# Kernel tuning notes

Hardware: AMD Instinct MI355X
Metric: run time of the kernel (lower is better)

The kernel has to match this reference:

```python
import jax, jax.numpy as jnp
import numpy as np

P = 8          # patch_num_in == patch_num_out
R = 16         # patch_resolution (pixels per patch side)
C = 2          # dim_channel
D = 512        # dim_token
NH = 8         # nhead
DFF = 2048     # dim_feedforward
L = 6          # num_layers
PAIRS = 5      # demo_num
BS = 8
HW = P * R     # 128
S = PAIRS * 2 * P * P  # 640 tokens
EPS = 1e-5


def _patchify(x):
    # x: (N, c, H, W) -> (N, P*P, c*R*R)
    N, c, H, W = x.shape
    x = x.reshape(N, c, P, R, P, R).transpose(0, 2, 4, 1, 3, 5)
    return x.reshape(N, P * P, c * R * R)


def _depatchify(x, c):
    # x: (N, P*P, c*R*R) -> (N, c, P*R, P*R)
    N = x.shape[0]
    x = x.reshape(N, P, P, c, R, R).transpose(0, 3, 1, 4, 2, 5)
    return x.reshape(N, c, P * R, P * R)


def _ln(x, s, b):
    mu = jnp.mean(x, axis=-1, keepdims=True)
    var = jnp.mean(jnp.square(x - mu), axis=-1, keepdims=True)
    return (x - mu) * jax.lax.rsqrt(var + EPS) * s + b


def _block_lowtri_additive_mask(seq_len):
    blk = jnp.arange(seq_len) // (P * P)  # alternating init/end blocks of size P*P
    allowed = blk[:, None] >= blk[None, :]
    return jnp.where(allowed, 0.0, -jnp.inf).astype(jnp.float32)


def setup_inputs() -> dict:
    key = jax.random.key(0)
    ks = jax.random.split(key, 20)
    s = 0.02
    f32 = jnp.float32
    inp = {
        "init": jax.random.normal(ks[0], (BS, PAIRS, C, HW, HW), f32),
        "end": jax.random.normal(ks[1], (BS, PAIRS, C, HW, HW), f32),
        "c_mask": jnp.ones((BS, C), dtype=bool),
        "pre_W": (jax.random.normal(ks[2], (D, C * R * R), f32) * s),
        "pre_b": jnp.zeros((D,), f32),
        "post_W": (jax.random.normal(ks[3], (C * R * R, D), f32) * s),
        "post_b": jnp.zeros((C * R * R,), f32),
        "patch_pos": jax.random.normal(ks[4], (P * P, D), f32),
        "func_pos": jax.random.normal(ks[5], (PAIRS * 2, D), f32),
        "Wqkv": (jax.random.normal(ks[6], (L, 3 * D, D), f32) * s),
        "bqkv": jnp.zeros((L, 3 * D), f32),
        "Wo": (jax.random.normal(ks[7], (L, D, D), f32) * s),
        "bo": jnp.zeros((L, D), f32),
        "ln1_s": jnp.ones((L, D), f32),
        "ln1_b": jnp.zeros((L, D), f32),
        "ln2_s": jnp.ones((L, D), f32),
        "ln2_b": jnp.zeros((L, D), f32),
        "W1": (jax.random.normal(ks[8], (L, DFF, D), f32) * s),
        "b1": jnp.zeros((L, DFF), f32),
        "W2": (jax.random.normal(ks[9], (L, D, DFF), f32) * s),
        "b2": jnp.zeros((L, D), f32),
    }
    return inp


def _forward(init, end, pre_W, pre_b, post_W, post_b, patch_pos, func_pos,
             Wqkv, bqkv, Wo, bo, ln1_s, ln1_b, ln2_s, ln2_b, W1, b1, W2, b2):
    bs, pairs = init.shape[0], init.shape[1]
    # interleave (init, end) per pair: (bs, pairs, 2, c, h, w)
    x = jnp.concatenate([init[:, :, None], end[:, :, None]], axis=2)
    f = x.reshape(-1, C, HW, HW)
    f = _patchify(f)                                    # (N, P*P, C*R*R)
    f = f @ pre_W.T + pre_b                             # (N, P*P, D)
    f = f + patch_pos                                   # patch pos encoding
    f = f.reshape(bs, pairs * 2, P * P, D)
    f = f + func_pos[: pairs * 2][None, :, None, :]     # func pos encoding
    seq = pairs * 2 * P * P
    f = f.reshape(bs, seq, D)

    amask = _block_lowtri_additive_mask(seq)            # (S, S) additive
    dh = D // NH
    scale = 1.0 / np.sqrt(dh).astype(np.float32)

    for l in range(L):
        qkv = f @ Wqkv[l].T + bqkv[l]                   # (bs, S, 3D)
        q, k, v = jnp.split(qkv, 3, axis=-1)
        q = q.reshape(bs, seq, NH, dh).transpose(0, 2, 1, 3)
        k = k.reshape(bs, seq, NH, dh).transpose(0, 2, 1, 3)
        v = v.reshape(bs, seq, NH, dh).transpose(0, 2, 1, 3)
        scores = jnp.einsum('bhqd,bhkd->bhqk', q, k) * scale + amask
        attn = jax.nn.softmax(scores, axis=-1)
        o = jnp.einsum('bhqk,bhkd->bhqd', attn, v)
        o = o.transpose(0, 2, 1, 3).reshape(bs, seq, D)
        o = o @ Wo[l].T + bo[l]
        f = _ln(f + o, ln1_s[l], ln1_b[l])              # post-norm (PyTorch default)
        ff = jax.nn.gelu(f @ W1[l].T + b1[l], approximate=False) @ W2[l].T + b2[l]
        f = _ln(f + ff, ln2_s[l], ln2_b[l])

    f = f.reshape(bs, pairs, 2, P * P, D)[:, :, 0]      # read prediction off init slots
    f = f @ post_W.T + post_b                           # (bs, pairs, P*P, C*R*R)
    f = f.reshape(bs * pairs, P * P, C * R * R)
    f = _depatchify(f, C)
    return f.reshape(bs, pairs, C, HW, HW)


def reference(init, end, c_mask, pre_W, pre_b, post_W, post_b, patch_pos, func_pos,
              Wqkv, bqkv, Wo, bo, ln1_s, ln1_b, ln2_s, ln2_b, W1, b1, W2, b2):
    # c_mask is unpacked but unused by the original forward
    return _forward(init, end, pre_W, pre_b, post_W, post_b, patch_pos, func_pos,
                    Wqkv, bqkv, Wo, bo, ln1_s, ln1_b, ln2_s, ln2_b, W1, b1, W2, b2)
```

## Files before the change

### kernel.cpp

```cpp
#include <hip/hip_runtime.h>
#include <hip/hip_bf16.h>

#define BSZ 8
#define PAIRS 5
#define NCH 2
#define HWP 128
#define PP 64
#define DIM 512
#define NHEAD 8
#define DHEAD 64
#define DFF 2048
#define NLAYER 6
#define SEQ 640
#define NTOK (BSZ * SEQ)
#define FIN 10
#define MPOST (BSZ * PAIRS * PP)

typedef unsigned short u16;
typedef __bf16 bf16_t;
typedef __attribute__((ext_vector_type(8))) __bf16 bf16x8;
typedef __attribute__((ext_vector_type(8))) unsigned short u16x8;
typedef __attribute__((ext_vector_type(4))) unsigned short u16x4;
typedef __attribute__((ext_vector_type(4))) float f32x4;
#define MFMA16(a, b, c) __builtin_amdgcn_mfma_f32_16x16x32_bf16(a, b, c, 0, 0, 0)

__device__ __forceinline__ u16 f2b(float x) {
  unsigned u = __float_as_uint(x);
  return (u16)((u + 0x7fffu + ((u >> 16) & 1u)) >> 16);
}

__device__ __forceinline__ float gelu_t(float x) {
  float y = 0.7978845608f * (x + 0.044715f * x * x * x);
  y = fminf(fmaxf(y, -10.f), 10.f);
  float e = __expf(2.f * y);
  return 0.5f * x * (1.f + (e - 1.f) / (e + 1.f));
}

__device__ __forceinline__ void dma16(const u16* g, void* l) {
  __builtin_amdgcn_global_load_lds(
      (const __attribute__((address_space(1))) void*)g,
      (__attribute__((address_space(3))) void*)l, 16, 0, 0);
}

template <int N> __device__ __forceinline__ void vwait() {
  if constexpr (N == 0) asm volatile("s_waitcnt vmcnt(0)" ::: "memory");
  else if constexpr (N == 2) asm volatile("s_waitcnt vmcnt(2)" ::: "memory");
  else if constexpr (N == 3) asm volatile("s_waitcnt vmcnt(3)" ::: "memory");
  else if constexpr (N == 4) asm volatile("s_waitcnt vmcnt(4)" ::: "memory");
  else if constexpr (N == 6) asm volatile("s_waitcnt vmcnt(6)" ::: "memory");
}

#define W_QKV (3 * DIM * DIM)
#define W_O (DIM * DIM)
#define W_1 (DFF * DIM)
#define OFF_O W_QKV
#define OFF_1 (W_QKV + W_O)
#define OFF_2 (W_QKV + W_O + W_1)
#define W_ALL (W_QKV + W_O + 2 * W_1)
#define PREPOST (2 * DIM * DIM)
#define N_CVT (PREPOST + NLAYER * W_ALL)

__global__ __launch_bounds__(256) void k_cvt_all(const float* __restrict__ preW,
                                                 const float* __restrict__ postW,
                                                 const float* __restrict__ wq,
                                                 const float* __restrict__ wo,
                                                 const float* __restrict__ w1,
                                                 const float* __restrict__ w2,
                                                 u16* __restrict__ dst) {
  size_t i = ((size_t)blockIdx.x * 256 + threadIdx.x) * 8;
  const float* src;
  size_t off;
  if (i < DIM * DIM) { src = preW; off = i; }
  else if (i < PREPOST) { src = postW; off = i - DIM * DIM; }
  else {
    size_t j = i - PREPOST;
    int l = (int)(j / W_ALL);
    size_t r = j - (size_t)l * W_ALL;
    if (r < OFF_O) { src = wq + (size_t)l * W_QKV; off = r; }
    else if (r < OFF_1) { src = wo + (size_t)l * W_O; off = r - OFF_O; }
    else if (r < OFF_2) { src = w1 + (size_t)l * W_1; off = r - OFF_1; }
    else { src = w2 + (size_t)l * W_1; off = r - OFF_2; }
  }
  float4 v0 = *(const float4*)(src + off);
  float4 v1 = *(const float4*)(src + off + 4);
  u16x8 o;
  o[0] = f2b(v0.x); o[1] = f2b(v0.y); o[2] = f2b(v0.z); o[3] = f2b(v0.w);
  o[4] = f2b(v1.x); o[5] = f2b(v1.y); o[6] = f2b(v1.z); o[7] = f2b(v1.w);
  *(u16x8*)(dst + i) = o;
}

__global__ __launch_bounds__(256) void k_patchify(const float* __restrict__ init,
                                                  const float* __restrict__ endp,
                                                  u16* __restrict__ A) {
  int i = blockIdx.x * 256 + threadIdx.x;
  int d = i & 511;
  int g = i >> 9;
  int p = g & 63;
  int fi = (g >> 6) % FIN;
  int b = g / SEQ;
  int e = fi & 1;
  int pr = fi >> 1;
  int c = d >> 8;
  int r1 = (d >> 4) & 15;
  int r2 = d & 15;
  int row = ((p >> 3) << 4) + r1;
  int col = ((p & 7) << 4) + r2;
  const float* src = e ? endp : init;
  size_t off = ((size_t)((b * PAIRS + pr) * NCH + c) << 14) + (size_t)row * HWP + col;
  A[i] = f2b(src[off]);
}

template <int BM, int NT, int MODE, int GATHER>
__global__ __launch_bounds__(256) void k_mma(const u16* __restrict__ A,
                                             const u16* __restrict__ B,
                                             const float* __restrict__ bias,
                                             u16* __restrict__ outB,
                                             float* __restrict__ outP,
                                             float* __restrict__ outF,
                                             const float* __restrict__ pp,
                                             const float* __restrict__ fp,
                                             int M, int N, int K, int act) {
  constexpr int FJ = NT / 32;
  constexpr int MI = BM / 32;
  constexpr int ACH = BM / 16;
  constexpr int NC = (BM / 16 + NT / 16) / 4;
  __shared__ __align__(16) bf16_t As[4][BM][32];
  __shared__ __align__(16) bf16_t Bs[4][NT][32];
  const int t = threadIdx.x;
  const int w = t >> 6, lane = t & 63, quad = lane >> 4, l16 = lane & 15;
  int bx = blockIdx.x, by = blockIdx.y;
  if ((gridDim.y & 7) == 0) {
    int lin = bx + gridDim.x * by;
    int xcd = lin & 7, slot = lin >> 3;
    int gx = gridDim.x;
    by = (gridDim.y >> 3) * xcd + slot / gx;
    bx = slot % gx;
  }
  const int row0 = by * BM, col0 = bx * NT;
  const int mB = (w & 1) * (BM / 2);
  const int nB = (w >> 1) * (NT / 2);

  const u16* aP[ACH];
#pragma unroll
  for (int c = 0; c < ACH; ++c) {
    int r = row0 + c * 16 + (lane >> 2);
    int g = r;
    if (GATHER) {
      int p = r & 63, pr = (r >> 6) % PAIRS, b = r / (PAIRS * PP);
      g = b * SEQ + pr * 128 + p;
    }
    aP[c] = A + (size_t)g * K + ((lane & 3) << 3);
  }
  const u16* bP = B + (size_t)(col0 + (lane >> 2)) * K + ((lane & 3) << 3);

  f32x4 acc[MI][FJ];
#pragma unroll
  for (int i = 0; i < MI; ++i)
#pragma unroll
    for (int j = 0; j < FJ; ++j) acc[i][j] = (f32x4){0.f, 0.f, 0.f, 0.f};

  auto stage = [&](int bu, int kk) {
#pragma unroll
    for (int s = 0; s < NC; ++s) {
      int c = NC * w + s;
      if (c < ACH) dma16(aP[c] + kk, &As[bu][c * 16][0]);
      else dma16(bP + (size_t)((c - ACH) * 16) * K + kk, &Bs[bu][(c - ACH) * 16][0]);
    }
  };

  const int iters = K >> 5;
  stage(0, 0);
  stage(1, 32);
  for (int it = 0; it < iters; ++it) {
    const int cur = it & 3;
    if (it + 2 < iters) stage((it + 2) & 3, (it + 2) << 5);
    if (it + 2 < iters) vwait<2 * NC>();
    else if (it + 1 < iters) vwait<NC>();
    else vwait<0>();
    asm volatile("s_barrier" ::: "memory");
    bf16x8 af[MI], bfr[FJ];
#pragma unroll
    for (int i = 0; i < MI; ++i)
      af[i] = *(const bf16x8*)&As[cur][mB + i * 16 + l16][quad * 8];
#pragma unroll
    for (int j = 0; j < FJ; ++j)
      bfr[j] = *(const bf16x8*)&Bs[cur][nB + j * 16 + l16][quad * 8];
#pragma unroll
    for (int i = 0; i < MI; ++i)
#pragma unroll
      for (int j = 0; j < FJ; ++j) acc[i][j] = MFMA16(af[i], bfr[j], acc[i][j]);
  }

#pragma unroll
  for (int i = 0; i < MI; ++i)
#pragma unroll
    for (int reg = 0; reg < 4; ++reg) {
      int m = row0 + mB + i * 16 + quad * 4 + reg;
#pragma unroll
      for (int j = 0; j < FJ; ++j) {
        int n = col0 + nB + j * 16 + l16;
        float v = acc[i][j][reg];
        if (MODE == 0) {
          v += bias[n];
          if (act) v = gelu_t(v);
          outB[(size_t)m * N + n] = f2b(v);
        } else if (MODE == 1) {
          outP[(size_t)m * N + n] = v;
        } else if (MODE == 2) {
          int p = m & 63, fi = (m >> 6) % FIN;
          v += bias[n] + pp[p * DIM + n] + fp[fi * DIM + n];
          outF[(size_t)m * N + n] = v;
          outB[(size_t)m * N + n] = f2b(v);
        } else {
          v += bias[n];
          int p = m & 63, pr = (m >> 6) % PAIRS, b = m / (PAIRS * PP);
          int c = n >> 8, r1 = (n >> 4) & 15, r2 = n & 15;
          int row = ((p >> 3) << 4) + r1, col = ((p & 7) << 4) + r2;
          size_t off = ((size_t)((b * PAIRS + pr) * NCH + c) << 14) +
                       (size_t)row * HWP + col;
          outF[off] = v;
        }
      }
    }
}

__global__ __launch_bounds__(256) void k_attn(const u16* __restrict__ qkv,
                                              u16* __restrict__ o, int qmul) {
  __shared__ bf16_t Ks[2][64][72];
  __shared__ bf16_t Vs[2][64][72];
  __shared__ bf16_t QPs[64][72];
  const int t = threadIdx.x;
  const int w = t >> 6, lane = t & 63, quad = lane >> 4, l16 = lane & 15;
  const int qblk = ((int)gridDim.x - 1 - (int)blockIdx.x) * qmul;
  const int h = blockIdx.y, b = blockIdx.z;
  const int q0 = qblk << 6;
  const u16* base = qkv + (size_t)b * SEQ * (3 * DIM);
  const int sr = t >> 2;
  const int sd = (t & 3) << 4;
  const int rowB = 3 * DIM;
  const int ntile = qblk + 1;
  {
    const u16* qp = base + (size_t)(q0 + sr) * rowB + h * DHEAD + sd;
    *(bf16x8*)&QPs[sr][sd] = *(const bf16x8*)(const void*)qp;
    *(bf16x8*)&QPs[sr][sd + 8] = *(const bf16x8*)(const void*)(qp + 8);
  }
  const u16* kp0 = base + (size_t)sr * rowB + DIM + h * DHEAD + sd;
  const u16* vp0 = base + (size_t)sr * rowB + 2 * DIM + h * DHEAD + sd;
  bf16x8 kR0 = *(const bf16x8*)(const void*)kp0;
  bf16x8 kR1 = *(const bf16x8*)(const void*)(kp0 + 8);
  bf16x8 vR0 = *(const bf16x8*)(const void*)vp0;
  bf16x8 vR1 = *(const bf16x8*)(const void*)(vp0 + 8);
  *(bf16x8*)&Ks[0][sr][sd] = kR0;
  *(bf16x8*)&Ks[0][sr][sd + 8] = kR1;
#pragma unroll
  for (int e = 0; e < 8; ++e) Vs[0][sd + e][sr] = vR0[e];
#pragma unroll
  for (int e = 0; e < 8; ++e) Vs[0][sd + 8 + e][sr] = vR1[e];
  __syncthreads();
  bf16x8 aQ0 = *(const bf16x8*)&QPs[w * 16 + l16][quad * 8];
  bf16x8 aQ1 = *(const bf16x8*)&QPs[w * 16 + l16][32 + quad * 8];
  f32x4 accO[4];
#pragma unroll
  for (int j = 0; j < 4; ++j) accO[j] = (f32x4){0.f, 0.f, 0.f, 0.f};
  float mSt[4] = {-1e30f, -1e30f, -1e30f, -1e30f};
  float lSt[4] = {0.f, 0.f, 0.f, 0.f};
  for (int kt = 0; kt < ntile; ++kt) {
    const int cur = kt & 1;
    if (kt > 0) __syncthreads();
    if (kt + 1 < ntile) {
      const u16* kp = kp0 + (size_t)(kt + 1) * 64 * rowB;
      const u16* vp = vp0 + (size_t)(kt + 1) * 64 * rowB;
      kR0 = *(const bf16x8*)(const void*)kp;
      kR1 = *(const bf16x8*)(const void*)(kp + 8);
      vR0 = *(const bf16x8*)(const void*)vp;
      vR1 = *(const bf16x8*)(const void*)(vp + 8);
    }
    f32x4 s[4];
#pragma unroll
    for (int j = 0; j < 4; ++j) {
      bf16x8 b0 = *(const bf16x8*)&Ks[cur][j * 16 + l16][quad * 8];
      bf16x8 b1 = *(const bf16x8*)&Ks[cur][j * 16 + l16][32 + quad * 8];
      s[j] = (f32x4){0.f, 0.f, 0.f, 0.f};
      s[j] = MFMA16(aQ0, b0, s[j]);
      s[j] = MFMA16(aQ1, b1, s[j]);
      s[j] *= 0.125f;
    }
#pragma unroll
    for (int reg = 0; reg < 4; ++reg) {
      float mx = fmaxf(fmaxf(s[0][reg], s[1][reg]), fmaxf(s[2][reg], s[3][reg]));
      mx = fmaxf(mx, __shfl_xor(mx, 1));
      mx = fmaxf(mx, __shfl_xor(mx, 2));
      mx = fmaxf(mx, __shfl_xor(mx, 4));
      mx = fmaxf(mx, __shfl_xor(mx, 8));
      float mNew = fmaxf(mSt[reg], mx);
      float alpha = __expf(mSt[reg] - mNew);
      mSt[reg] = mNew;
      float rs = 0.f;
#pragma unroll
      for (int j = 0; j < 4; ++j) {
        float p = __expf(s[j][reg] - mNew);
        s[j][reg] = p;
        rs += p;
      }
      rs += __shfl_xor(rs, 1);
      rs += __shfl_xor(rs, 2);
      rs += __shfl_xor(rs, 4);
      rs += __shfl_xor(rs, 8);
      lSt[reg] = lSt[reg] * alpha + rs;
#pragma unroll
      for (int j = 0; j < 4; ++j) accO[j][reg] *= alpha;
    }
#pragma unroll
    for (int j = 0; j < 4; ++j)
#pragma unroll
      for (int reg = 0; reg < 4; ++reg)
        *(u16*)&QPs[w * 16 + quad * 4 + reg][j * 16 + l16] = f2b(s[j][reg]);
    if (kt + 1 < ntile) {
      const int nxt = cur ^ 1;
      *(bf16x8*)&Ks[nxt][sr][sd] = kR0;
      *(bf16x8*)&Ks[nxt][sr][sd + 8] = kR1;
#pragma unroll
      for (int e = 0; e < 8; ++e) Vs[nxt][sd + e][sr] = vR0[e];
#pragma unroll
      for (int e = 0; e < 8; ++e) Vs[nxt][sd + 8 + e][sr] = vR1[e];
    }
    bf16x8 aP0 = *(const bf16x8*)&QPs[w * 16 + l16][quad * 8];
    bf16x8 aP1 = *(const bf16x8*)&QPs[w * 16 + l16][32 + quad * 8];
#pragma unroll
    for (int jd = 0; jd < 4; ++jd) {
      bf16x8 b0 = *(const bf16x8*)&Vs[cur][jd * 16 + l16][quad * 8];
      bf16x8 b1 = *(const bf16x8*)&Vs[cur][jd * 16 + l16][32 + quad * 8];
      accO[jd] = MFMA16(aP0, b0, accO[jd]);
      accO[jd] = MFMA16(aP1, b1, accO[jd]);
    }
  }
#pragma unroll
  for (int reg = 0; reg < 4; ++reg) {
    float inv = 1.0f / lSt[reg];
    int row = q0 + w * 16 + quad * 4 + reg;
#pragma unroll
    for (int jd = 0; jd < 4; ++jd)
      o[((size_t)(b * SEQ + row)) * DIM + h * DHEAD + jd * 16 + l16] =
          f2b(accO[jd][reg] * inv);
  }
}

template <int GIN>
__global__ __launch_bounds__(256) void k_red_ln(const float* __restrict__ part,
                                                const float* __restrict__ bias,
                                                const float* __restrict__ f_in,
                                                float* __restrict__ f_out,
                                                u16* __restrict__ fb_out,
                                                const float* __restrict__ s,
                                                const float* __restrict__ bvec) {
  const int t = threadIdx.x;
  const int half = t >> 7;
  const int r = blockIdx.x * 2 + half;
  const int c = (t & 127) * 4;
  int g = r;
  if (GIN) {
    int p = r & 63, pr = (r >> 6) % PAIRS, b = r / (PAIRS * PP);
    g = b * SEQ + pr * 128 + p;
  }
  float4 x = *(const float4*)(f_in + (size_t)g * DIM + c);
  float4 pa = *(const float4*)(part + (size_t)r * DIM + c);
  float4 bi = *(const float4*)(bias + c);
  x.x += pa.x + bi.x; x.y += pa.y + bi.y; x.z += pa.z + bi.z; x.w += pa.w + bi.w;
  float sum = x.x + x.y + x.z + x.w;
  float sq = x.x * x.x + x.y * x.y + x.z * x.z + x.w * x.w;
#pragma unroll
  for (int off = 32; off; off >>= 1) {
    sum += __shfl_xor(sum, off);
    sq += __shfl_xor(sq, off);
  }
  __shared__ float rs[4], rq[4];
  const int w = t >> 6, lane = t & 63;
  if (lane == 0) { rs[w] = sum; rq[w] = sq; }
  __syncthreads();
  float tot = rs[half * 2] + rs[half * 2 + 1];
  float tq2 = rq[half * 2] + rq[half * 2 + 1];
  float mu = tot * (1.0f / 512.0f);
  float var = tq2 * (1.0f / 512.0f) - mu * mu;
  float rstd = rsqrtf(var + 1e-5f);
  float4 sv = *(const float4*)(s + c);
  float4 bv = *(const float4*)(bvec + c);
  float4 o;
  o.x = (x.x - mu) * rstd * sv.x + bv.x;
  o.y = (x.y - mu) * rstd * sv.y + bv.y;
  o.z = (x.z - mu) * rstd * sv.z + bv.z;
  o.w = (x.w - mu) * rstd * sv.w + bv.w;
  *(float4*)(f_out + (size_t)r * DIM + c) = o;
  u16x4 ob;
  ob[0] = f2b(o.x); ob[1] = f2b(o.y); ob[2] = f2b(o.z); ob[3] = f2b(o.w);
  *(u16x4*)(fb_out + (size_t)r * DIM + c) = ob;
}

extern "C" void kernel_launch(void* const* d_in, const int* in_sizes, int n_in,
                              void* d_out, int out_size, void* d_ws, size_t ws_size,
                              hipStream_t stream) {
  const float* init = (const float*)d_in[0];
  const float* endp = (const float*)d_in[1];
  const float* pre_W = (const float*)d_in[3];
  const float* pre_b = (const float*)d_in[4];
  const float* post_W = (const float*)d_in[5];
  const float* post_b = (const float*)d_in[6];
  const float* patch_pos = (const float*)d_in[7];
  const float* func_pos = (const float*)d_in[8];
  const float* Wqkv = (const float*)d_in[9];
  const float* bqkv = (const float*)d_in[10];
  const float* Wo = (const float*)d_in[11];
  const float* bo = (const float*)d_in[12];
  const float* ln1_s = (const float*)d_in[13];
  const float* ln1_b = (const float*)d_in[14];
  const float* ln2_s = (const float*)d_in[15];
  const float* ln2_b = (const float*)d_in[16];
  const float* W1 = (const float*)d_in[17];
  const float* b1 = (const float*)d_in[18];
  const float* W2 = (const float*)d_in[19];
  const float* b2 = (const float*)d_in[20];
  float* out = (float*)d_out;

  char* p = (char*)d_ws;
  float* buf_f = (float*)p;    p += (size_t)NTOK * DIM * 4;
  u16* buf_fb = (u16*)p;       p += (size_t)NTOK * DIM * 2;
  u16* buf_attn = (u16*)p;     p += (size_t)NTOK * DIM * 2;
  u16* shared_b = (u16*)p;     p += (size_t)NTOK * DFF * 2;
  u16* wAll = (u16*)p;         p += (size_t)N_CVT * 2;
  float* partial = (float*)p;  p += (size_t)NTOK * DIM * 4;
  float* buf_fc = (float*)p;   p += (size_t)MPOST * DIM * 4;
  u16* buf_fbc = (u16*)p;      p += (size_t)MPOST * DIM * 2;
  u16* buf_patch = shared_b;
  u16* buf_qkv = shared_b;
  u16* buf_hid = shared_b;
  u16* wPre = wAll;
  u16* wPost = wAll + DIM * DIM;
  u16* wL = wAll + PREPOST;

  dim3 blk(256);
  const int elems = NTOK * DIM;

  k_cvt_all<<<N_CVT / (256 * 8), blk, 0, stream>>>(pre_W, post_W, Wqkv, Wo, W1, W2,
                                                   wAll);
  k_patchify<<<elems / 256, blk, 0, stream>>>(init, endp, buf_patch);
  k_mma<64, 64, 2, 0><<<dim3(8, 80), blk, 0, stream>>>(
      buf_patch, wPre, pre_b, buf_fb, nullptr, buf_f, patch_pos, func_pos,
      NTOK, DIM, DIM, 0);

  for (int l = 0; l < NLAYER; ++l) {
    u16* wB = wL + (size_t)l * W_ALL;
    k_mma<64, 128, 0, 0><<<dim3(12, 80), blk, 0, stream>>>(
        buf_fb, wB, bqkv + (size_t)l * 3 * DIM, buf_qkv, nullptr, nullptr, nullptr,
        nullptr, NTOK, 3 * DIM, DIM, 0);
    if (l < NLAYER - 1) {
      k_attn<<<dim3(SEQ / 64, NHEAD, BSZ), blk, 0, stream>>>(buf_qkv, buf_attn, 1);
      k_mma<64, 64, 1, 0><<<dim3(8, 80), blk, 0, stream>>>(
          buf_attn, wB + OFF_O, nullptr, nullptr, partial, nullptr, nullptr, nullptr,
          NTOK, DIM, DIM, 0);
      k_red_ln<0><<<NTOK / 2, blk, 0, stream>>>(partial, bo + (size_t)l * DIM,
                                                buf_f, buf_f, buf_fb,
                                                ln1_s + (size_t)l * DIM,
                                                ln1_b + (size_t)l * DIM);
      k_mma<64, 128, 0, 0><<<dim3(16, 80), blk, 0, stream>>>(
          buf_fb, wB + OFF_1, b1 + (size_t)l * DFF, buf_hid, nullptr, nullptr,
          nullptr, nullptr, NTOK, DFF, DIM, 1);
      k_mma<64, 64, 1, 0><<<dim3(8, 80), blk, 0, stream>>>(
          buf_hid, wB + OFF_2, nullptr, nullptr, partial, nullptr, nullptr, nullptr,
          NTOK, DIM, DFF, 0);
      k_red_ln<0><<<NTOK / 2, blk, 0, stream>>>(partial, b2 + (size_t)l * DIM,
                                                buf_f, buf_f, buf_fb,
                                                ln2_s + (size_t)l * DIM,
                                                ln2_b + (size_t)l * DIM);
    } else {
      k_attn<<<dim3(SEQ / 128, NHEAD, BSZ), blk, 0, stream>>>(buf_qkv, buf_attn, 2);
      k_mma<64, 64, 1, 1><<<dim3(8, 40), blk, 0, stream>>>(
          buf_attn, wB + OFF_O, nullptr, nullptr, partial, nullptr, nullptr, nullptr,
          MPOST, DIM, DIM, 0);
      k_red_ln<1><<<MPOST / 2, blk, 0, stream>>>(partial, bo + (size_t)l * DIM,
                                                 buf_f, buf_fc, buf_fbc,
                                                 ln1_s + (size_t)l * DIM,
                                                 ln1_b + (size_t)l * DIM);
      k_mma<64, 128, 0, 0><<<dim3(16, 40), blk, 0, stream>>>(
          buf_fbc, wB + OFF_1, b1 + (size_t)l * DFF, buf_hid, nullptr, nullptr,
          nullptr, nullptr, MPOST, DFF, DIM, 1);
      k_mma<64, 64, 1, 0><<<dim3(8, 40), blk, 0, stream>>>(
          buf_hid, wB + OFF_2, nullptr, nullptr, partial, nullptr, nullptr, nullptr,
          MPOST, DIM, DFF, 0);
      k_red_ln<0><<<MPOST / 2, blk, 0, stream>>>(partial, b2 + (size_t)l * DIM,
                                                 buf_fc, buf_fc, buf_fbc,
                                                 ln2_s + (size_t)l * DIM,
                                                 ln2_b + (size_t)l * DIM);
    }
  }

  k_mma<64, 64, 3, 0><<<dim3(8, 40), blk, 0, stream>>>(
      buf_fbc, wPost, post_b, nullptr, nullptr, out, nullptr, nullptr,
      MPOST, DIM, DIM, 0);
}
```

Measured before the change: 868.4 us.

## Use warp-private LDS staging in GEMM to drop block barriers

The GEMM kernel is restructured so that each wavefront DMA-loads its own 32-row A and 32-row B slices into a private LDS region. Because no wavefront reads another's data, the per-k-step s_barrier can be removed. The tile shape is also fixed at 64x64, so the QKV and FFN1 launches now use twice as many blocks. The cost is that A and B rows are fetched twice per block, which gives up intra-block reuse and adds L2 and global traffic.

```diff
diff --git a/kernel.cpp b/kernel.cpp
--- a/kernel.cpp
+++ b/kernel.cpp
@@ -44,10 +44,8 @@
 
 template <int N> __device__ __forceinline__ void vwait() {
   if constexpr (N == 0) asm volatile("s_waitcnt vmcnt(0)" ::: "memory");
-  else if constexpr (N == 2) asm volatile("s_waitcnt vmcnt(2)" ::: "memory");
-  else if constexpr (N == 3) asm volatile("s_waitcnt vmcnt(3)" ::: "memory");
   else if constexpr (N == 4) asm volatile("s_waitcnt vmcnt(4)" ::: "memory");
-  else if constexpr (N == 6) asm volatile("s_waitcnt vmcnt(6)" ::: "memory");
+  else if constexpr (N == 8) asm volatile("s_waitcnt vmcnt(8)" ::: "memory");
 }
 
 #define W_QKV (3 * DIM * DIM)
@@ -110,7 +108,7 @@
   A[i] = f2b(src[off]);
 }
 
-template <int BM, int NT, int MODE, int GATHER>
+template <int MODE, int GATHER>
 __global__ __launch_bounds__(256) void k_mma(const u16* __restrict__ A,
                                              const u16* __restrict__ B,
                                              const float* __restrict__ bias,
@@ -120,12 +118,7 @@
                                              const float* __restrict__ pp,
                                              const float* __restrict__ fp,
                                              int M, int N, int K, int act) {
-  constexpr int FJ = NT / 32;
-  constexpr int MI = BM / 32;
-  constexpr int ACH = BM / 16;
-  constexpr int NC = (BM / 16 + NT / 16) / 4;
-  __shared__ __align__(16) bf16_t As[4][BM][32];
-  __shared__ __align__(16) bf16_t Bs[4][NT][32];
+  __shared__ __align__(16) bf16_t S[4][4][4][16][32];
   const int t = threadIdx.x;
   const int w = t >> 6, lane = t & 63, quad = lane >> 4, l16 = lane & 15;
   int bx = blockIdx.x, by = blockIdx.y;
@@ -136,14 +129,14 @@
     by = (gridDim.y >> 3) * xcd + slot / gx;
     bx = slot % gx;
   }
-  const int row0 = by * BM, col0 = bx * NT;
-  const int mB = (w & 1) * (BM / 2);
-  const int nB = (w >> 1) * (NT / 2);
-
-  const u16* aP[ACH];
-#pragma unroll
-  for (int c = 0; c < ACH; ++c) {
-    int r = row0 + c * 16 + (lane >> 2);
+  const int row0 = by * 64, col0 = bx * 64;
+  const int mB = (w & 1) * 32;
+  const int nB = (w >> 1) * 32;
+
+  const u16* aP[2];
+#pragma unroll
+  for (int c = 0; c < 2; ++c) {
+    int r = row0 + mB + c * 16 + (lane >> 2);
     int g = r;
     if (GATHER) {
       int p = r & 63, pr = (r >> 6) % PAIRS, b = r / (PAIRS * PP);
@@ -151,21 +144,19 @@
     }
     aP[c] = A + (size_t)g * K + ((lane & 3) << 3);
   }
-  const u16* bP = B + (size_t)(col0 + (lane >> 2)) * K + ((lane & 3) << 3);
-
-  f32x4 acc[MI][FJ];
-#pragma unroll
-  for (int i = 0; i < MI; ++i)
-#pragma unroll
-    for (int j = 0; j < FJ; ++j) acc[i][j] = (f32x4){0.f, 0.f, 0.f, 0.f};
+  const u16* bP = B + (size_t)(col0 + nB + (lane >> 2)) * K + ((lane & 3) << 3);
+
+  f32x4 acc[2][2];
+#pragma unroll
+  for (int i = 0; i < 2; ++i)
+#pragma unroll
+    for (int j = 0; j < 2; ++j) acc[i][j] = (f32x4){0.f, 0.f, 0.f, 0.f};
 
   auto stage = [&](int bu, int kk) {
-#pragma unroll
-    for (int s = 0; s < NC; ++s) {
-      int c = NC * w + s;
-      if (c < ACH) dma16(aP[c] + kk, &As[bu][c * 16][0]);
-      else dma16(bP + (size_t)((c - ACH) * 16) * K + kk, &Bs[bu][(c - ACH) * 16][0]);
-    }
+    dma16(aP[0] + kk, &S[bu][w][0][0][0]);
+    dma16(aP[1] + kk, &S[bu][w][1][0][0]);
+    dma16(bP + kk, &S[bu][w][2][0][0]);
+    dma16(bP + (size_t)16 * K + kk, &S[bu][w][3][0][0]);
   };
 
   const int iters = K >> 5;
@@ -174,30 +165,29 @@
   for (int it = 0; it < iters; ++it) {
     const int cur = it & 3;
     if (it + 2 < iters) stage((it + 2) & 3, (it + 2) << 5);
-    if (it + 2 < iters) vwait<2 * NC>();
-    else if (it + 1 < iters) vwait<NC>();
+    if (it + 2 < iters) vwait<8>();
+    else if (it + 1 < iters) vwait<4>();
     else vwait<0>();
-    asm volatile("s_barrier" ::: "memory");
-    bf16x8 af[MI], bfr[FJ];
-#pragma unroll
-    for (int i = 0; i < MI; ++i)
-      af[i] = *(const bf16x8*)&As[cur][mB + i * 16 + l16][quad * 8];
-#pragma unroll
-    for (int j = 0; j < FJ; ++j)
-      bfr[j] = *(const bf16x8*)&Bs[cur][nB + j * 16 + l16][quad * 8];
-#pragma unroll
-    for (int i = 0; i < MI; ++i)
-#pragma unroll
-      for (int j = 0; j < FJ; ++j) acc[i][j] = MFMA16(af[i], bfr[j], acc[i][j]);
-  }
-
-#pragma unroll
-  for (int i = 0; i < MI; ++i)
+    bf16x8 af[2], bfr[2];
+#pragma unroll
+    for (int i = 0; i < 2; ++i)
+      af[i] = *(const bf16x8*)&S[cur][w][i][l16][quad * 8];
+#pragma unroll
+    for (int j = 0; j < 2; ++j)
+      bfr[j] = *(const bf16x8*)&S[cur][w][2 + j][l16][quad * 8];
+#pragma unroll
+    for (int i = 0; i < 2; ++i)
+#pragma unroll
+      for (int j = 0; j < 2; ++j) acc[i][j] = MFMA16(af[i], bfr[j], acc[i][j]);
+  }
+
+#pragma unroll
+  for (int i = 0; i < 2; ++i)
 #pragma unroll
     for (int reg = 0; reg < 4; ++reg) {
       int m = row0 + mB + i * 16 + quad * 4 + reg;
 #pragma unroll
-      for (int j = 0; j < FJ; ++j) {
+      for (int j = 0; j < 2; ++j) {
         int n = col0 + nB + j * 16 + l16;
         float v = acc[i][j][reg];
         if (MODE == 0) {
@@ -442,28 +432,28 @@
   k_cvt_all<<<N_CVT / (256 * 8), blk, 0, stream>>>(pre_W, post_W, Wqkv, Wo, W1, W2,
                                                    wAll);
   k_patchify<<<elems / 256, blk, 0, stream>>>(init, endp, buf_patch);
-  k_mma<64, 64, 2, 0><<<dim3(8, 80), blk, 0, stream>>>(
+  k_mma<2, 0><<<dim3(8, 80), blk, 0, stream>>>(
       buf_patch, wPre, pre_b, buf_fb, nullptr, buf_f, patch_pos, func_pos,
       NTOK, DIM, DIM, 0);
 
   for (int l = 0; l < NLAYER; ++l) {
     u16* wB = wL + (size_t)l * W_ALL;
-    k_mma<64, 128, 0, 0><<<dim3(12, 80), blk, 0, stream>>>(
+    k_mma<0, 0><<<dim3(24, 80), blk, 0, stream>>>(
         buf_fb, wB, bqkv + (size_t)l * 3 * DIM, buf_qkv, nullptr, nullptr, nullptr,
         nullptr, NTOK, 3 * DIM, DIM, 0);
     if (l < NLAYER - 1) {
       k_attn<<<dim3(SEQ / 64, NHEAD, BSZ), blk, 0, stream>>>(buf_qkv, buf_attn, 1);
-      k_mma<64, 64, 1, 0><<<dim3(8, 80), blk, 0, stream>>>(
+      k_mma<1, 0><<<dim3(8, 80), blk, 0, stream>>>(
           buf_attn, wB + OFF_O, nullptr, nullptr, partial, nullptr, nullptr, nullptr,
           NTOK, DIM, DIM, 0);
       k_red_ln<0><<<NTOK / 2, blk, 0, stream>>>(partial, bo + (size_t)l * DIM,
                                                 buf_f, buf_f, buf_fb,
                                                 ln1_s + (size_t)l * DIM,
                                                 ln1_b + (size_t)l * DIM);
-      k_mma<64, 128, 0, 0><<<dim3(16, 80), blk, 0, stream>>>(
+      k_mma<0, 0><<<dim3(32, 80), blk, 0, stream>>>(
           buf_fb, wB + OFF_1, b1 + (size_t)l * DFF, buf_hid, nullptr, nullptr,
           nullptr, nullptr, NTOK, DFF, DIM, 1);
-      k_mma<64, 64, 1, 0><<<dim3(8, 80), blk, 0, stream>>>(
+      k_mma<1, 0><<<dim3(8, 80), blk, 0, stream>>>(
           buf_hid, wB + OFF_2, nullptr, nullptr, partial, nullptr, nullptr, nullptr,
           NTOK, DIM, DFF, 0);
       k_red_ln<0><<<NTOK / 2, blk, 0, stream>>>(partial, b2 + (size_t)l * DIM,
@@ -472,17 +462,17 @@
                                                 ln2_b + (size_t)l * DIM);
     } else {
       k_attn<<<dim3(SEQ / 128, NHEAD, BSZ), blk, 0, stream>>>(buf_qkv, buf_attn, 2);
-      k_mma<64, 64, 1, 1><<<dim3(8, 40), blk, 0, stream>>>(
+      k_mma<1, 1><<<dim3(8, 40), blk, 0, stream>>>(
           buf_attn, wB + OFF_O, nullptr, nullptr, partial, nullptr, nullptr, nullptr,
           MPOST, DIM, DIM, 0);
       k_red_ln<1><<<MPOST / 2, blk, 0, stream>>>(partial, bo + (size_t)l * DIM,
                                                  buf_f, buf_fc, buf_fbc,
                                                  ln1_s + (size_t)l * DIM,
                                                  ln1_b + (size_t)l * DIM);
-      k_mma<64, 128, 0, 0><<<dim3(16, 40), blk, 0, stream>>>(
+      k_mma<0, 0><<<dim3(32, 40), blk, 0, stream>>>(
           buf_fbc, wB + OFF_1, b1 + (size_t)l * DFF, buf_hid, nullptr, nullptr,
           nullptr, nullptr, MPOST, DFF, DIM, 1);
-      k_mma<64, 64, 1, 0><<<dim3(8, 40), blk, 0, stream>>>(
+      k_mma<1, 0><<<dim3(8, 40), blk, 0, stream>>>(
           buf_hid, wB + OFF_2, nullptr, nullptr, partial, nullptr, nullptr, nullptr,
           MPOST, DIM, DFF, 0);
       k_red_ln<0><<<MPOST / 2, blk, 0, stream>>>(partial, b2 + (size_t)l * DIM,
@@ -492,7 +482,7 @@
     }
   }
 
-  k_mma<64, 64, 3, 0><<<dim3(8, 40), blk, 0, stream>>>(
+  k_mma<3, 0><<<dim3(8, 40), blk, 0, stream>>>(
       buf_fbc, wPost, post_b, nullptr, nullptr, out, nullptr, nullptr,
       MPOST, DIM, DIM, 0);
 }
```

Result: slower. 997.0 us (+14.8%).
